# Performance work log

Measured on AMD Instinct MI355X. Metric: run time of the kernel, lower is better.

Reference implementation:

```python
import jax, jax.numpy as jnp
import numpy as np

NUM_GROUPS = 512
GROUP_SIZE = 32
GROUP_RADIUS = 0.2
K_ORIGINAL = 5 * GROUP_SIZE  # ball_query oversampling factor from the source


def setup_inputs() -> dict:
    key = jax.random.key(0)
    k1, k2 = jax.random.split(key)
    B, N, C = 8, 16384, 4
    points = jax.random.normal(k1, (B, N, C), dtype=jnp.float32)
    # valid lengths in [N//2, N) so the lengths-masking path is exercised
    lengths = (N // 2 + jax.random.randint(k2, (B,), 0, N // 2)).astype(jnp.int32)
    return {"points": points, "lengths": lengths}


def _sample_farthest_points(xyz, lengths, K):
    # xyz: (B,N,3) float, lengths: (B,) int -> centers (B,K,3)
    B, N, _ = xyz.shape
    n_idx = jnp.arange(N)

    def per_batch(pts, length):
        valid = n_idx < length

        def step(carry, _):
            mindist, cur = carry
            d = jnp.sum((pts - pts[cur]) ** 2, axis=-1)  # (N,)
            mindist = jnp.where(valid, jnp.minimum(mindist, d), -jnp.inf)
            nxt = jnp.argmax(mindist).astype(jnp.int32)
            return (mindist, nxt), cur

        mindist0 = jnp.where(valid, jnp.inf, -jnp.inf)
        # deterministic start at index 0 (source uses random_start_point=True)
        (_, _), sel = jax.lax.scan(step, (mindist0, jnp.int32(0)), None, length=K)
        return pts[sel]

    return jax.vmap(per_batch)(xyz, lengths)


def _ball_query(centers, xyz, lengths, K, radius):
    # returns first-K (by point index, matching pytorch3d ball_query) indices
    # within radius; -1 padding. centers (B,G,3), xyz (B,N,3) -> idx (B,G,K)
    B, G, _ = centers.shape
    N = xyz.shape[1]
    d2 = jnp.sum((centers[:, :, None, :] - xyz[:, None, :, :]) ** 2, axis=-1)  # (B,G,N)
    valid = (jnp.arange(N) < lengths[:, None])[:, None, :]  # (B,1,N)
    mask = (d2 < radius * radius) & valid
    # score N-n > 0 iff in ball; top_k picks smallest indices first (in order)
    score = jnp.where(mask, N - jnp.arange(N, dtype=jnp.int32), jnp.int32(-1))
    vals, _ = jax.lax.top_k(score, K)
    return jnp.where(vals > 0, N - vals, -1)  # (B,G,K)


def _select_topk_by_energy(points, idx, K_new):
    # points (B,N,C), idx (B,G,K_orig) with -1 invalid -> (B,G,K_new)
    B, G, _ = idx.shape
    N = points.shape[1]
    invalid = idx == -1
    idxc = jnp.maximum(idx, 0)
    energies = jnp.broadcast_to(points[:, None, :, 3], (B, G, N))
    e = jnp.take_along_axis(energies, idxc, axis=2)  # (B,G,K_orig)
    e = jnp.where(invalid, -jnp.inf, e)
    top_e, top_i = jax.lax.top_k(e, K_new)
    topk_idx = jnp.take_along_axis(idx, top_i, axis=2)
    return jnp.where(top_e == -jnp.inf, -1, topk_idx)


def _masked_gather(points, idx):
    # points (B,N,C), idx (B,G,K); -1 -> gathered value 0.0 (pytorch3d semantics)
    B, G, K = idx.shape
    C = points.shape[-1]
    valid = idx >= 0
    flat = jnp.maximum(idx, 0).reshape(B, G * K)
    g = jnp.take_along_axis(points, flat[:, :, None], axis=1).reshape(B, G, K, C)
    return jnp.where(valid[..., None], g, 0.0)


def _forward(points, lengths):
    xyz = points[:, :, :3]
    centers = _sample_farthest_points(xyz, lengths, NUM_GROUPS)  # (B,G,3)
    idx = _ball_query(centers, xyz, lengths, K_ORIGINAL, GROUP_RADIUS)
    idx = _select_topk_by_energy(points, idx, GROUP_SIZE)  # (B,G,K)
    # fill_empty_indices: replace -1 with first index of the group
    first = idx[:, :, :1]
    idx = jnp.where(idx == -1, first, idx)
    groups = _masked_gather(points, idx)  # (B,G,K,C)
    groups = jnp.concatenate(
        [groups[..., :3] - centers[:, :, None, :], groups[..., 3:]], axis=-1
    )
    groups = groups / GROUP_RADIUS
    return groups, centers


def reference(points, lengths):
    return _forward(points, lengths)
```

## Files before the change

### kernel.cpp

```cpp
#include <hip/hip_runtime.h>

constexpr int B_ = 8;
constexpr int N_ = 16384;
constexpr int NG = 512;
constexpr int GS = 32;
constexpr int KORIG = 160;
constexpr int TPB = 1024;
constexpr int PPT = 16;
#define R2 0.04f
#define RADIUS 0.2f

typedef __attribute__((ext_vector_type(2))) float f32x2;

__device__ __forceinline__ unsigned f32_ord(float f) {
  unsigned u = __float_as_uint(f);
  return (u & 0x80000000u) ? ~u : (u | 0x80000000u);
}

__device__ __forceinline__ f32x2 pk_add(f32x2 a, f32x2 b) {
  f32x2 d;
  asm("v_pk_add_f32 %0, %1, %2" : "=v"(d) : "v"(a), "v"(b));
  return d;
}
__device__ __forceinline__ f32x2 pk_mul(f32x2 a, f32x2 b) {
  f32x2 d;
  asm("v_pk_mul_f32 %0, %1, %2" : "=v"(d) : "v"(a), "v"(b));
  return d;
}

template <int CTRL>
__device__ __forceinline__ float dpp_fmax(float v) {
  int o = __builtin_amdgcn_update_dpp(0, __float_as_int(v), CTRL, 0xF, 0xF, true);
  return fmaxf(v, __int_as_float(o));
}
__device__ __forceinline__ float wave_fmax(float v) {
  v = dpp_fmax<0xB1>(v);
  v = dpp_fmax<0x4E>(v);
  v = dpp_fmax<0x141>(v);
  v = dpp_fmax<0x140>(v);
  v = fmaxf(v, __int_as_float(__builtin_amdgcn_ds_swizzle(__float_as_int(v), 0x401F)));
  v = fmaxf(v, __shfl_xor(v, 32, 64));
  return v;
}
__device__ __forceinline__ float group16_fmax(float v) {
  v = dpp_fmax<0xB1>(v);
  v = dpp_fmax<0x4E>(v);
  v = dpp_fmax<0x141>(v);
  v = dpp_fmax<0x140>(v);
  return v;
}

__global__ __attribute__((amdgpu_flat_work_group_size(1024, 1024),
                          amdgpu_waves_per_eu(4, 4)))
void fps_kernel(const float4* __restrict__ p4,
                const int* __restrict__ lengths,
                float* __restrict__ centers) {
#pragma clang fp contract(off)
  const int b = blockIdx.x;
  const int t = threadIdx.x;
  const int lane = t & 63;
  const int wid = t >> 6;
  const int len = lengths[b];
  const float4* bp = p4 + (size_t)b * N_;
  const float INF = __builtin_inff();

  __shared__ float pubf[2][16];
  __shared__ int pubi[2][16];

  f32x2 x2[8], y2[8], z2[8], m2[8];
#pragma unroll
  for (int p = 0; p < 8; ++p) {
    const int i0 = t * PPT + 2 * p;
    float4 a = bp[i0];
    float4 c = bp[i0 + 1];
    x2[p] = (f32x2){a.x, c.x};
    y2[p] = (f32x2){a.y, c.y};
    z2[p] = (f32x2){a.z, c.z};
    m2[p].x = (i0 < len) ? INF : -INF;
    m2[p].y = (i0 + 1 < len) ? INF : -INF;
  }

  float4 c0 = bp[0];
  float cx = c0.x, cy = c0.y, cz = c0.z;
  if (t == 0) {
    size_t o = (size_t)b * NG * 3;
    centers[o] = cx; centers[o + 1] = cy; centers[o + 2] = cz;
  }

  for (int k = 0; k < NG - 1; ++k) {
    const f32x2 mcx = {-cx, -cx};
    const f32x2 mcy = {-cy, -cy};
    const f32x2 mcz = {-cz, -cz};
#pragma unroll
    for (int p = 0; p < 8; ++p) {
      f32x2 xx = pk_add(x2[p], mcx);
      f32x2 yy = pk_add(y2[p], mcy);
      f32x2 zz = pk_add(z2[p], mcz);
      f32x2 xs = pk_mul(xx, xx);
      f32x2 ys = pk_mul(yy, yy);
      f32x2 s1 = pk_add(xs, ys);
      f32x2 zs = pk_mul(zz, zz);
      f32x2 d2 = pk_add(s1, zs);
      m2[p].x = fminf(m2[p].x, d2.x);
      m2[p].y = fminf(m2[p].y, d2.y);
    }
    float pm[8];
#pragma unroll
    for (int i = 0; i < 8; ++i) pm[i] = fmaxf(m2[i].x, m2[i].y);
    float b4[4];
#pragma unroll
    for (int i = 0; i < 4; ++i) b4[i] = fmaxf(pm[2 * i], pm[2 * i + 1]);
    float b2[2] = {fmaxf(b4[0], b4[1]), fmaxf(b4[2], b4[3])};
    const float sm = fmaxf(b2[0], b2[1]);

    const bool i1 = (b2[0] != sm);
    const float aL4 = i1 ? b4[2] : b4[0];
    const bool i2 = (aL4 != sm);
    const float pmL = i1 ? (i2 ? pm[6] : pm[4]) : (i2 ? pm[2] : pm[0]);
    const bool i3 = (pmL != sm);
    const int jp = ((int)i1 << 2) | ((int)i2 << 1) | (int)i3;
    const float mlo =
        i1 ? (i2 ? (i3 ? m2[7].x : m2[6].x) : (i3 ? m2[5].x : m2[4].x))
           : (i2 ? (i3 ? m2[3].x : m2[2].x) : (i3 ? m2[1].x : m2[0].x));
    const bool blo = (mlo != sm);
    const int gidx = t * PPT + jp * 2 + (int)blo;

    const float wmax = wave_fmax(sm);
    const unsigned long long att = __ballot(sm == wmax);
    const int wl = __ffsll(att) - 1;
    if (lane == wl) {
      pubf[k & 1][wid] = wmax;
      pubi[k & 1][wid] = gidx;
    }
    __syncthreads();

    const float pw = pubf[k & 1][lane & 15];
    const int pi = pubi[k & 1][lane & 15];
    const float kmax = group16_fmax(pw);
    const unsigned long long bal = __ballot(pw == kmax);
    const int grp = lane & 48;
    const int src = grp + (__ffsll((bal >> grp) & 0xFFFFull) - 1);
    const int gsel = __shfl(pi, src, 64);
    const int snxt = __builtin_amdgcn_readfirstlane(gsel);
    const float4 c = bp[snxt];
    cx = c.x; cy = c.y; cz = c.z;

    if (t == 0) {
      size_t o = ((size_t)b * NG + (k + 1)) * 3;
      centers[o] = cx; centers[o + 1] = cy; centers[o + 2] = cz;
    }
  }
}

__global__ __launch_bounds__(64) void group_kernel(const float4* __restrict__ p4,
                                                   const int* __restrict__ lengths,
                                                   const float* __restrict__ centers,
                                                   float4* __restrict__ outg) {
#pragma clang fp contract(off)
  const int gid = blockIdx.x;
  const int b = gid >> 9;
  const int lane = threadIdx.x;
  const int len = lengths[b];
  const float4* bp = p4 + (size_t)b * N_;
  const float cx = centers[(size_t)gid * 3 + 0];
  const float cy = centers[(size_t)gid * 3 + 1];
  const float cz = centers[(size_t)gid * 3 + 2];

  __shared__ int cand[KORIG];
  int M = 0;
  for (int cb = 0; cb < N_ && M < KORIG; cb += 256) {
#pragma unroll
    for (int q = 0; q < 4; ++q) {
      const int i = cb + q * 64 + lane;
      float4 p = bp[i];
      float dx = p.x - cx;
      float dy = p.y - cy;
      float dz = p.z - cz;
      float d2 = dx * dx + dy * dy + dz * dz;
      const bool pred = (i < len) && (d2 < R2);
      unsigned long long mb = __ballot(pred);
      if (pred) {
        int pos = M + (int)__popcll(mb & ((1ull << lane) - 1ull));
        if (pos < KORIG) cand[pos] = i;
      }
      M += (int)__popcll(mb);
    }
  }
  if (M > KORIG) M = KORIG;
  __syncthreads();

  const unsigned long long SENT = ~0ull;
  unsigned long long key0 = SENT, key1 = SENT, key2 = SENT;
  {
    int c0 = lane, c1 = lane + 64, c2 = lane + 128;
    if (c0 < M) { int i = cand[c0]; key0 = ((unsigned long long)(~f32_ord(bp[i].w)) << 32) | (unsigned)i; }
    if (c1 < M) { int i = cand[c1]; key1 = ((unsigned long long)(~f32_ord(bp[i].w)) << 32) | (unsigned)i; }
    if (c2 < M) { int i = cand[c2]; key2 = ((unsigned long long)(~f32_ord(bp[i].w)) << 32) | (unsigned)i; }
  }

  int mysel = -1;
  for (int j = 0; j < GS; ++j) {
    unsigned long long kmin = key0 < key1 ? key0 : key1;
    if (key2 < kmin) kmin = key2;
#pragma unroll
    for (int off = 32; off > 0; off >>= 1) {
      unsigned long long o = __shfl_xor(kmin, off, 64);
      if (o < kmin) kmin = o;
    }
    if (kmin == SENT) break;
    if (lane == j) mysel = (int)(unsigned)kmin;
    if (key0 == kmin) key0 = SENT;
    if (key1 == kmin) key1 = SENT;
    if (key2 == kmin) key2 = SENT;
  }

  const int first = __shfl(mysel, 0, 64);
  if (lane < GS) {
    int idx = (mysel < 0) ? first : mysel;
    float4 o;
    if (idx >= 0) {
      float4 p = bp[idx];
      o.x = (p.x - cx) / RADIUS;
      o.y = (p.y - cy) / RADIUS;
      o.z = (p.z - cz) / RADIUS;
      o.w = p.w / RADIUS;
    } else {
      o.x = (0.0f - cx) / RADIUS;
      o.y = (0.0f - cy) / RADIUS;
      o.z = (0.0f - cz) / RADIUS;
      o.w = 0.0f;
    }
    outg[(size_t)gid * GS + lane] = o;
  }
}

extern "C" void kernel_launch(void* const* d_in, const int* in_sizes, int n_in,
                              void* d_out, int out_size, void* d_ws, size_t ws_size,
                              hipStream_t stream) {
  const float4* pts = (const float4*)d_in[0];
  const int* lengths = (const int*)d_in[1];
  float* out = (float*)d_out;
  float* centers = out + (size_t)B_ * NG * GS * 4;
  float4* groups = (float4*)out;

  fps_kernel<<<B_, TPB, 0, stream>>>(pts, lengths, centers);
  group_kernel<<<B_ * NG, 64, 0, stream>>>(pts, lengths, centers, groups);
}
```

Baseline: 893.3 us.

## Fuse FPS and grouping into one persistent kernel with progress flags

Merges the farthest-point-sampling kernel and the ball-query/grouping kernel into a single launch. Eight blocks run FPS and publish each new center with a release store to a per-batch progress counter. 256 extra blocks of 16 waves each spin on that counter and process groups as soon as their center is ready. This overlaps the grouping work with the serial FPS loop instead of running it afterwards. It depends on all blocks being co-resident, since otherwise consumer blocks could occupy CUs and delay the FPS blocks. The spinning waves also compete for resources with the FPS blocks.

```diff
diff --git a/kernel.cpp b/kernel.cpp
--- a/kernel.cpp
+++ b/kernel.cpp
@@ -7,6 +7,8 @@
 constexpr int KORIG = 160;
 constexpr int TPB = 1024;
 constexpr int PPT = 16;
+constexpr int NFPS = 8;
+constexpr int NGRPBLK = 256;
 #define R2 0.04f
 #define RADIUS 0.2f
 
@@ -50,22 +52,116 @@
   return v;
 }
 
+__global__ void prog_init(unsigned* prog) { prog[threadIdx.x] = 0u; }
+
 __global__ __attribute__((amdgpu_flat_work_group_size(1024, 1024),
                           amdgpu_waves_per_eu(4, 4)))
-void fps_kernel(const float4* __restrict__ p4,
-                const int* __restrict__ lengths,
-                float* __restrict__ centers) {
+void fused_kernel(const float4* __restrict__ p4,
+                  const int* __restrict__ lengths,
+                  float* __restrict__ centers,
+                  float4* __restrict__ outg,
+                  unsigned* __restrict__ prog) {
 #pragma clang fp contract(off)
-  const int b = blockIdx.x;
   const int t = threadIdx.x;
   const int lane = t & 63;
   const int wid = t >> 6;
+
+  __shared__ float pubf[2][16];
+  __shared__ int pubi[2][16];
+  __shared__ int candw[16][KORIG];
+
+  if (blockIdx.x >= NFPS) {
+    const int G = ((int)blockIdx.x - NFPS) * 16 + wid;
+    const int b = G >> 9;
+    const int g = G & 511;
+    const float4* bp = p4 + (size_t)b * N_;
+    const int len = lengths[b];
+
+    while (__hip_atomic_load(&prog[b], __ATOMIC_ACQUIRE,
+                             __HIP_MEMORY_SCOPE_AGENT) <= (unsigned)g) {
+      __builtin_amdgcn_s_sleep(32);
+    }
+    const unsigned* cbits = (const unsigned*)(centers + (size_t)(b * NG + g) * 3);
+    const float cx = __uint_as_float(__hip_atomic_load(
+        &cbits[0], __ATOMIC_RELAXED, __HIP_MEMORY_SCOPE_AGENT));
+    const float cy = __uint_as_float(__hip_atomic_load(
+        &cbits[1], __ATOMIC_RELAXED, __HIP_MEMORY_SCOPE_AGENT));
+    const float cz = __uint_as_float(__hip_atomic_load(
+        &cbits[2], __ATOMIC_RELAXED, __HIP_MEMORY_SCOPE_AGENT));
+
+    int* cand = candw[wid];
+    int M = 0;
+    for (int cb = 0; cb < N_ && M < KORIG; cb += 256) {
+#pragma unroll
+      for (int q = 0; q < 4; ++q) {
+        const int i = cb + q * 64 + lane;
+        float4 p = bp[i];
+        float dx = p.x - cx;
+        float dy = p.y - cy;
+        float dz = p.z - cz;
+        float d2 = dx * dx + dy * dy + dz * dz;
+        const bool pred = (i < len) && (d2 < R2);
+        unsigned long long mb = __ballot(pred);
+        if (pred) {
+          int pos = M + (int)__popcll(mb & ((1ull << lane) - 1ull));
+          if (pos < KORIG) cand[pos] = i;
+        }
+        M += (int)__popcll(mb);
+      }
+    }
+    if (M > KORIG) M = KORIG;
+
+    const unsigned long long SENT = ~0ull;
+    unsigned long long key0 = SENT, key1 = SENT, key2 = SENT;
+    {
+      int c0 = lane, c1 = lane + 64, c2 = lane + 128;
+      if (c0 < M) { int i = cand[c0]; key0 = ((unsigned long long)(~f32_ord(bp[i].w)) << 32) | (unsigned)i; }
+      if (c1 < M) { int i = cand[c1]; key1 = ((unsigned long long)(~f32_ord(bp[i].w)) << 32) | (unsigned)i; }
+      if (c2 < M) { int i = cand[c2]; key2 = ((unsigned long long)(~f32_ord(bp[i].w)) << 32) | (unsigned)i; }
+    }
+
+    int mysel = -1;
+    for (int j = 0; j < GS; ++j) {
+      unsigned long long kmin = key0 < key1 ? key0 : key1;
+      if (key2 < kmin) kmin = key2;
+#pragma unroll
+      for (int off = 32; off > 0; off >>= 1) {
+        unsigned long long o = __shfl_xor(kmin, off, 64);
+        if (o < kmin) kmin = o;
+      }
+      if (kmin == SENT) break;
+      if (lane == j) mysel = (int)(unsigned)kmin;
+      if (key0 == kmin) key0 = SENT;
+      if (key1 == kmin) key1 = SENT;
+      if (key2 == kmin) key2 = SENT;
+    }
+
+    const int first = __shfl(mysel, 0, 64);
+    if (lane < GS) {
+      int idx = (mysel < 0) ? first : mysel;
+      float4 o;
+      if (idx >= 0) {
+        float4 p = bp[idx];
+        o.x = (p.x - cx) / RADIUS;
+        o.y = (p.y - cy) / RADIUS;
+        o.z = (p.z - cz) / RADIUS;
+        o.w = p.w / RADIUS;
+      } else {
+        o.x = (0.0f - cx) / RADIUS;
+        o.y = (0.0f - cy) / RADIUS;
+        o.z = (0.0f - cz) / RADIUS;
+        o.w = 0.0f;
+      }
+      outg[(size_t)G * GS + lane] = o;
+    }
+    return;
+  }
+
+  const int b = blockIdx.x;
   const int len = lengths[b];
   const float4* bp = p4 + (size_t)b * N_;
   const float INF = __builtin_inff();
-
-  __shared__ float pubf[2][16];
-  __shared__ int pubi[2][16];
+  unsigned* cOut = (unsigned*)(centers + (size_t)b * NG * 3);
 
   f32x2 x2[8], y2[8], z2[8], m2[8];
 #pragma unroll
@@ -83,8 +179,10 @@
   float4 c0 = bp[0];
   float cx = c0.x, cy = c0.y, cz = c0.z;
   if (t == 0) {
-    size_t o = (size_t)b * NG * 3;
-    centers[o] = cx; centers[o + 1] = cy; centers[o + 2] = cz;
+    __hip_atomic_store(&cOut[0], __float_as_uint(cx), __ATOMIC_RELAXED, __HIP_MEMORY_SCOPE_AGENT);
+    __hip_atomic_store(&cOut[1], __float_as_uint(cy), __ATOMIC_RELAXED, __HIP_MEMORY_SCOPE_AGENT);
+    __hip_atomic_store(&cOut[2], __float_as_uint(cz), __ATOMIC_RELAXED, __HIP_MEMORY_SCOPE_AGENT);
+    __hip_atomic_store(&prog[b], 1u, __ATOMIC_RELEASE, __HIP_MEMORY_SCOPE_AGENT);
   }
 
   for (int k = 0; k < NG - 1; ++k) {
@@ -146,91 +244,12 @@
     cx = c.x; cy = c.y; cz = c.z;
 
     if (t == 0) {
-      size_t o = ((size_t)b * NG + (k + 1)) * 3;
-      centers[o] = cx; centers[o + 1] = cy; centers[o + 2] = cz;
-    }
-  }
-}
-
-__global__ __launch_bounds__(64) void group_kernel(const float4* __restrict__ p4,
-                                                   const int* __restrict__ lengths,
-                                                   const float* __restrict__ centers,
-                                                   float4* __restrict__ outg) {
-#pragma clang fp contract(off)
-  const int gid = blockIdx.x;
-  const int b = gid >> 9;
-  const int lane = threadIdx.x;
-  const int len = lengths[b];
-  const float4* bp = p4 + (size_t)b * N_;
-  const float cx = centers[(size_t)gid * 3 + 0];
-  const float cy = centers[(size_t)gid * 3 + 1];
-  const float cz = centers[(size_t)gid * 3 + 2];
-
-  __shared__ int cand[KORIG];
-  int M = 0;
-  for (int cb = 0; cb < N_ && M < KORIG; cb += 256) {
-#pragma unroll
-    for (int q = 0; q < 4; ++q) {
-      const int i = cb + q * 64 + lane;
-      float4 p = bp[i];
-      float dx = p.x - cx;
-      float dy = p.y - cy;
-      float dz = p.z - cz;
-      float d2 = dx * dx + dy * dy + dz * dz;
-      const bool pred = (i < len) && (d2 < R2);
-      unsigned long long mb = __ballot(pred);
-      if (pred) {
-        int pos = M + (int)__popcll(mb & ((1ull << lane) - 1ull));
-        if (pos < KORIG) cand[pos] = i;
-      }
-      M += (int)__popcll(mb);
-    }
-  }
-  if (M > KORIG) M = KORIG;
-  __syncthreads();
-
-  const unsigned long long SENT = ~0ull;
-  unsigned long long key0 = SENT, key1 = SENT, key2 = SENT;
-  {
-    int c0 = lane, c1 = lane + 64, c2 = lane + 128;
-    if (c0 < M) { int i = cand[c0]; key0 = ((unsigned long long)(~f32_ord(bp[i].w)) << 32) | (unsigned)i; }
-    if (c1 < M) { int i = cand[c1]; key1 = ((unsigned long long)(~f32_ord(bp[i].w)) << 32) | (unsigned)i; }
-    if (c2 < M) { int i = cand[c2]; key2 = ((unsigned long long)(~f32_ord(bp[i].w)) << 32) | (unsigned)i; }
-  }
-
-  int mysel = -1;
-  for (int j = 0; j < GS; ++j) {
-    unsigned long long kmin = key0 < key1 ? key0 : key1;
-    if (key2 < kmin) kmin = key2;
-#pragma unroll
-    for (int off = 32; off > 0; off >>= 1) {
-      unsigned long long o = __shfl_xor(kmin, off, 64);
-      if (o < kmin) kmin = o;
-    }
-    if (kmin == SENT) break;
-    if (lane == j) mysel = (int)(unsigned)kmin;
-    if (key0 == kmin) key0 = SENT;
-    if (key1 == kmin) key1 = SENT;
-    if (key2 == kmin) key2 = SENT;
-  }
-
-  const int first = __shfl(mysel, 0, 64);
-  if (lane < GS) {
-    int idx = (mysel < 0) ? first : mysel;
-    float4 o;
-    if (idx >= 0) {
-      float4 p = bp[idx];
-      o.x = (p.x - cx) / RADIUS;
-      o.y = (p.y - cy) / RADIUS;
-      o.z = (p.z - cz) / RADIUS;
-      o.w = p.w / RADIUS;
-    } else {
-      o.x = (0.0f - cx) / RADIUS;
-      o.y = (0.0f - cy) / RADIUS;
-      o.z = (0.0f - cz) / RADIUS;
-      o.w = 0.0f;
-    }
-    outg[(size_t)gid * GS + lane] = o;
+      unsigned* co = cOut + (size_t)(k + 1) * 3;
+      __hip_atomic_store(&co[0], __float_as_uint(cx), __ATOMIC_RELAXED, __HIP_MEMORY_SCOPE_AGENT);
+      __hip_atomic_store(&co[1], __float_as_uint(cy), __ATOMIC_RELAXED, __HIP_MEMORY_SCOPE_AGENT);
+      __hip_atomic_store(&co[2], __float_as_uint(cz), __ATOMIC_RELAXED, __HIP_MEMORY_SCOPE_AGENT);
+      __hip_atomic_store(&prog[b], (unsigned)(k + 2), __ATOMIC_RELEASE, __HIP_MEMORY_SCOPE_AGENT);
+    }
   }
 }
 
@@ -242,7 +261,9 @@
   float* out = (float*)d_out;
   float* centers = out + (size_t)B_ * NG * GS * 4;
   float4* groups = (float4*)out;
-
-  fps_kernel<<<B_, TPB, 0, stream>>>(pts, lengths, centers);
-  group_kernel<<<B_ * NG, 64, 0, stream>>>(pts, lengths, centers, groups);
-}
+  unsigned* prog = (unsigned*)d_ws;
+
+  prog_init<<<1, B_, 0, stream>>>(prog);
+  fused_kernel<<<NFPS + NGRPBLK, TPB, 0, stream>>>(pts, lengths, centers,
+                                                   groups, prog);
+}
```

Result: slower. 1.204 ms (+34.7%).
